# Performance work log

Hardware: AMD Instinct MI355X
Metric: run time of the kernel (lower is better)

Reference implementation:

```python
import jax, jax.numpy as jnp
import numpy as np

WINDOW = 11
POLY = 3
HALF = WINDOW // 2


def _savgol_matrices():
    # Central FIR coefficients: fit degree-POLY poly to window centered at 0,
    # evaluate at 0. y[n] = sum_k c[k] * x[n - HALF + k]  (cross-correlation).
    pos = np.arange(-HALF, HALF + 1, dtype=np.float64)
    A = pos[:, None] ** np.arange(POLY + 1)[None, :]          # [W, P+1]
    c = np.linalg.pinv(A)[0]                                   # [W]
    # Edge handling (scipy mode='interp'): fit poly to first WINDOW samples at
    # positions 0..W-1, evaluate at positions 0..HALF-1. E: [HALF, W].
    V = np.arange(WINDOW, dtype=np.float64)[:, None] ** np.arange(POLY + 1)[None, :]
    T = np.arange(HALF, dtype=np.float64)[:, None] ** np.arange(POLY + 1)[None, :]
    E = T @ np.linalg.pinv(V)                                  # [HALF, W]
    return c, E

_C_NP, _E_NP = _savgol_matrices()


def setup_inputs() -> dict:
    key = jax.random.key(0)
    x = jax.random.normal(key, (64, 16, 65536), dtype=jnp.float32)
    return {"x": x}


def reference(x) -> jnp.ndarray:
    B, C, L = x.shape
    c = jnp.asarray(_C_NP, x.dtype)                 # [W] central FIR taps
    E = jnp.asarray(_E_NP, x.dtype)                 # [HALF, W] edge fit matrix
    # Interior: valid cross-correlation with the savgol taps.
    xr = x.reshape(B * C, 1, L)
    k = c.reshape(1, 1, WINDOW)                     # (out_ch, in_ch, W)
    interior = jax.lax.conv_general_dilated(
        xr, k, window_strides=(1,), padding='VALID'
    ).reshape(B, C, L - WINDOW + 1)
    # Left edge: polynomial extrapolation from the first WINDOW samples.
    left = jnp.einsum('hw,bcw->bch', E, x[..., :WINDOW])       # [B,C,HALF]
    # Right edge: by symmetry, fit the reversed tail and reverse the result.
    right = jnp.einsum('hw,bcw->bch', E, x[..., ::-1][..., :WINDOW])[..., ::-1]
    return jnp.concatenate([left, interior, right], axis=-1)
```

## Files before the change

### kernel.cpp

```cpp
#include <hip/hip_runtime.h>
#include <math.h>

#define WINDOW 11
#define POLY   3
#define HALF   5
#define TILE   2048
#define TPB    256
#define EPT    8

struct SgCoef {
    float c[WINDOW];
    float E[HALF][WINDOW];
};


static void invert4(const double M[4][4], double inv[4][4]) {
    double a[4][8];
    for (int i = 0; i < 4; ++i) {
        for (int j = 0; j < 4; ++j) { a[i][j] = M[i][j]; a[i][j + 4] = (i == j) ? 1.0 : 0.0; }
    }
    for (int col = 0; col < 4; ++col) {
        int piv = col;
        for (int r = col + 1; r < 4; ++r)
            if (fabs(a[r][col]) > fabs(a[piv][col])) piv = r;
        if (piv != col)
            for (int j = 0; j < 8; ++j) { double t = a[col][j]; a[col][j] = a[piv][j]; a[piv][j] = t; }
        double d = a[col][col];
        for (int j = 0; j < 8; ++j) a[col][j] /= d;
        for (int r = 0; r < 4; ++r) {
            if (r == col) continue;
            double f = a[r][col];
            for (int j = 0; j < 8; ++j) a[r][j] -= f * a[col][j];
        }
    }
    for (int i = 0; i < 4; ++i)
        for (int j = 0; j < 4; ++j) inv[i][j] = a[i][j + 4];
}

static SgCoef compute_coef() {
    SgCoef co;
    double A[WINDOW][4];
    for (int i = 0; i < WINDOW; ++i) {
        double p = (double)(i - HALF), v = 1.0;
        for (int j = 0; j < 4; ++j) { A[i][j] = v; v *= p; }
    }
    double N[4][4] = {};
    for (int i = 0; i < 4; ++i)
        for (int j = 0; j < 4; ++j) {
            double s = 0;
            for (int r = 0; r < WINDOW; ++r) s += A[r][i] * A[r][j];
            N[i][j] = s;
        }
    double Ninv[4][4];
    invert4(N, Ninv);
    for (int w = 0; w < WINDOW; ++w) {
        double s = 0;
        for (int j = 0; j < 4; ++j) s += Ninv[0][j] * A[w][j];
        co.c[w] = (float)s;
    }
    double V[WINDOW][4];
    for (int i = 0; i < WINDOW; ++i) {
        double p = (double)i, v = 1.0;
        for (int j = 0; j < 4; ++j) { V[i][j] = v; v *= p; }
    }
    double NV[4][4] = {};
    for (int i = 0; i < 4; ++i)
        for (int j = 0; j < 4; ++j) {
            double s = 0;
            for (int r = 0; r < WINDOW; ++r) s += V[r][i] * V[r][j];
            NV[i][j] = s;
        }
    double NVinv[4][4];
    invert4(NV, NVinv);
    for (int h = 0; h < HALF; ++h) {
        double T[4]; double v = 1.0;
        for (int j = 0; j < 4; ++j) { T[j] = v; v *= (double)h; }
        for (int w = 0; w < WINDOW; ++w) {
            double s = 0;
            for (int j = 0; j < 4; ++j) {
                double pv = 0;
                for (int m = 0; m < 4; ++m) pv += NVinv[j][m] * V[w][m];
                s += T[j] * pv;
            }
            co.E[h][w] = (float)s;
        }
    }
    return co;
}


__global__ __launch_bounds__(TPB) void savgol_kernel(
    const float* __restrict__ x, float* __restrict__ out,
    SgCoef coef, int L, int tiles_per_row)
{
    __shared__ float lds[TILE + 16];

    const int t    = threadIdx.x;
    const int tile = blockIdx.x;
    const int row  = blockIdx.y;
    const long long rowoff = (long long)row * (long long)L;
    const int s = tile * TILE;
    const float* __restrict__ xr  = x + rowoff;
    float* __restrict__       outr = out + rowoff;

    const int NCHUNK = (TILE + 16) / 4;
    for (int chunk = t; chunk < NCHUNK; chunk += TPB) {
        int gbase = s - 8 + chunk * 4;
        float4 v;
        if (gbase >= 0 && gbase + 3 < L) {
            v = *reinterpret_cast<const float4*>(xr + gbase);
        } else {
            float vv[4];
            #pragma unroll
            for (int q = 0; q < 4; ++q) {
                int g = gbase + q;
                vv[q] = (g >= 0 && g < L) ? xr[g] : 0.0f;
            }
            v = make_float4(vv[0], vv[1], vv[2], vv[3]);
        }
        *reinterpret_cast<float4*>(&lds[chunk * 4]) = v;
    }
    __syncthreads();

    const bool first = (tile == 0);
    const bool last  = (tile == tiles_per_row - 1);

    #pragma unroll
    for (int j = 0; j < EPT; ++j) {
        const int nl = t + j * TPB;
        const int n  = s + nl;
        float acc = 0.0f;
        #pragma unroll
        for (int k = 0; k < WINDOW; ++k)
            acc = fmaf(coef.c[k], lds[nl + 3 + k], acc);
        float val = acc;
        if (first && nl < HALF) {
            float a = 0.0f;
            #pragma unroll
            for (int w = 0; w < WINDOW; ++w)
                a = fmaf(coef.E[nl][w], lds[w + 8], a);
            val = a;
        } else if (last && nl >= TILE - HALF) {
            int h = (L - 1) - n;
            float a = 0.0f;
            #pragma unroll
            for (int w = 0; w < WINDOW; ++w)
                a = fmaf(coef.E[h][w], lds[(TILE + 7) - w], a);
            val = a;
        }
        outr[n] = val;
    }
}


extern "C" void kernel_launch(void* const* d_in, const int* in_sizes, int n_in,
                              void* d_out, int out_size, void* d_ws, size_t ws_size,
                              hipStream_t stream) {
    (void)d_ws; (void)ws_size; (void)n_in;
    const float* x = (const float*)d_in[0];
    float* out = (float*)d_out;

    const int L = 65536;
    const int rows = in_sizes[0] / L;
    const int tiles_per_row = L / TILE;

    SgCoef coef = compute_coef();

    dim3 grid(tiles_per_row, rows);
    dim3 block(TPB);
    savgol_kernel<<<grid, block, 0, stream>>>(x, out, coef, L, tiles_per_row);
}
```

Measured before the change: 97.67 us.

## Replace LDS tiling with per-thread register windows and vectorized stores

Drops the shared-memory tile and barrier. Each thread loads a contiguous 32-float window straight from global memory with float4 loads and computes 16 consecutive outputs from registers, then writes them with float4 stores. Tile size doubles to 4096 elements per block. The cost is redundant global loads of the halo: 32 floats are read per 16 outputs, which mostly hits cache. Per-thread strided accesses are also less coalesced than the old lane-contiguous pattern.

```diff
diff --git a/kernel.cpp b/kernel.cpp
--- a/kernel.cpp
+++ b/kernel.cpp
@@ -4,9 +4,9 @@
 #define WINDOW 11
 #define POLY   3
 #define HALF   5
-#define TILE   2048
+#define EPT    16
 #define TPB    256
-#define EPT    8
+#define TILE   (EPT * TPB)
 
 struct SgCoef {
     float c[WINDOW];
@@ -89,74 +89,84 @@
 }
 
 
-__global__ __launch_bounds__(TPB) void savgol_kernel(
+__global__ __launch_bounds__(TPB) void savgol_reg_kernel(
     const float* __restrict__ x, float* __restrict__ out,
     SgCoef coef, int L, int tiles_per_row)
 {
-    __shared__ float lds[TILE + 16];
-
     const int t    = threadIdx.x;
     const int tile = blockIdx.x;
     const int row  = blockIdx.y;
     const long long rowoff = (long long)row * (long long)L;
-    const int s = tile * TILE;
-    const float* __restrict__ xr  = x + rowoff;
+    const float* __restrict__ xr   = x + rowoff;
     float* __restrict__       outr = out + rowoff;
 
-    const int NCHUNK = (TILE + 16) / 4;
-    for (int chunk = t; chunk < NCHUNK; chunk += TPB) {
-        int gbase = s - 8 + chunk * 4;
-        float4 v;
-        if (gbase >= 0 && gbase + 3 < L) {
-            v = *reinterpret_cast<const float4*>(xr + gbase);
-        } else {
-            float vv[4];
-            #pragma unroll
-            for (int q = 0; q < 4; ++q) {
-                int g = gbase + q;
-                vv[q] = (g >= 0 && g < L) ? xr[g] : 0.0f;
-            }
-            v = make_float4(vv[0], vv[1], vv[2], vv[3]);
+    const int s    = tile * TILE;
+    const int base = s + EPT * t - 8;
+
+    float v[32];
+    const bool oob_lo = (base < 0);
+    const bool oob_hi = (base + 31 >= L);
+
+    if (!oob_lo && !oob_hi) {
+        const float4* p = reinterpret_cast<const float4*>(xr + base);
+        #pragma unroll
+        for (int i = 0; i < 8; ++i) {
+            float4 q = p[i];
+            v[4 * i + 0] = q.x; v[4 * i + 1] = q.y;
+            v[4 * i + 2] = q.z; v[4 * i + 3] = q.w;
         }
-        *reinterpret_cast<float4*>(&lds[chunk * 4]) = v;
+    } else {
+        #pragma unroll
+        for (int i = 0; i < 32; ++i) {
+            int g = base + i;
+            g = g < 0 ? 0 : (g > L - 1 ? L - 1 : g);
+            v[i] = xr[g];
+        }
     }
-    __syncthreads();
 
-    const bool first = (tile == 0);
-    const bool last  = (tile == tiles_per_row - 1);
-
+    float o[EPT];
     #pragma unroll
     for (int j = 0; j < EPT; ++j) {
-        const int nl = t + j * TPB;
-        const int n  = s + nl;
         float acc = 0.0f;
         #pragma unroll
         for (int k = 0; k < WINDOW; ++k)
-            acc = fmaf(coef.c[k], lds[nl + 3 + k], acc);
-        float val = acc;
-        if (first && nl < HALF) {
+            acc = fmaf(coef.c[k], v[j + 3 + k], acc);
+        o[j] = acc;
+    }
+
+    if (tile == 0 && t == 0) {
+        #pragma unroll
+        for (int h = 0; h < HALF; ++h) {
             float a = 0.0f;
             #pragma unroll
             for (int w = 0; w < WINDOW; ++w)
-                a = fmaf(coef.E[nl][w], lds[w + 8], a);
-            val = a;
-        } else if (last && nl >= TILE - HALF) {
-            int h = (L - 1) - n;
+                a = fmaf(coef.E[h][w], v[w + 8], a);
+            o[h] = a;
+        }
+    }
+    if (tile == tiles_per_row - 1 && t == TPB - 1) {
+        #pragma unroll
+        for (int j = EPT - HALF; j < EPT; ++j) {
+            const int h = (EPT - 1) - j;
             float a = 0.0f;
             #pragma unroll
             for (int w = 0; w < WINDOW; ++w)
-                a = fmaf(coef.E[h][w], lds[(TILE + 7) - w], a);
-            val = a;
+                a = fmaf(coef.E[h][w], v[23 - w], a);
+            o[j] = a;
         }
-        outr[n] = val;
     }
+
+    float4* po = reinterpret_cast<float4*>(outr + s + EPT * t);
+    #pragma unroll
+    for (int q = 0; q < 4; ++q)
+        po[q] = make_float4(o[4 * q], o[4 * q + 1], o[4 * q + 2], o[4 * q + 3]);
 }
 
 
 extern "C" void kernel_launch(void* const* d_in, const int* in_sizes, int n_in,
                               void* d_out, int out_size, void* d_ws, size_t ws_size,
                               hipStream_t stream) {
-    (void)d_ws; (void)ws_size; (void)n_in;
+    (void)d_ws; (void)ws_size; (void)n_in; (void)out_size;
     const float* x = (const float*)d_in[0];
     float* out = (float*)d_out;
 
@@ -168,5 +178,5 @@
 
     dim3 grid(tiles_per_row, rows);
     dim3 block(TPB);
-    savgol_kernel<<<grid, block, 0, stream>>>(x, out, coef, L, tiles_per_row);
+    savgol_reg_kernel<<<grid, block, 0, stream>>>(x, out, coef, L, tiles_per_row);
 }
```

Result: slower. 129.1 us (+32.2%).
